# Kernel optimization log

Hardware: AMD Instinct MI355X
Metric: run time of the kernel (lower is better)

## Reference

```python
import jax, jax.numpy as jnp
import numpy as np

B, T, J, C, H = 16, 448, 448, 1024, 16
HD = C // H
NEG_INF = float('-inf')


def _layernorm(x, g, b, eps=1e-5):
    mu = jnp.mean(x, axis=-1, keepdims=True)
    var = jnp.var(x, axis=-1, keepdims=True)
    return (x - mu) * jax.lax.rsqrt(var + eps) * g + b


def _heads(x):
    # [B, S, C] -> [B, H, S, HD]
    Bv, S, _ = x.shape
    return x.reshape(Bv, S, H, HD).transpose(0, 2, 1, 3)


def _merge(x):
    # [B, H, S, HD] -> [B, S, C]
    Bv, _, S, _ = x.shape
    return x.transpose(0, 2, 1, 3).reshape(Bv, S, C)


def setup_inputs() -> dict:
    key = jax.random.key(0)
    ks = jax.random.split(key, 16)
    s = 0.02
    return {
        'tgt': jax.random.normal(ks[0], (B, T, C), jnp.float32),
        'src': jax.random.normal(ks[1], (B, J, C), jnp.float32),
        'sa_wqkv': jax.random.normal(ks[2], (C, 3 * C), jnp.float32) * s,
        'sa_wproj': jax.random.normal(ks[3], (C, C), jnp.float32) * s,
        'sa_bproj': jnp.zeros((C,), jnp.float32),
        'ed_wkv': jax.random.normal(ks[4], (C, 2 * C), jnp.float32) * s,
        'ed_wq': jax.random.normal(ks[5], (C, C), jnp.float32) * s,
        'ed_wproj': jax.random.normal(ks[6], (C, C), jnp.float32) * s,
        'ed_bproj': jnp.zeros((C,), jnp.float32),
        'ff_w1': jax.random.normal(ks[7], (C, 4 * C), jnp.float32) * s,
        'ff_b1': jnp.zeros((4 * C,), jnp.float32),
        'ff_w2': jax.random.normal(ks[8], (4 * C, C), jnp.float32) * s,
        'ff_b2': jnp.zeros((C,), jnp.float32),
        'ln1_g': jnp.ones((C,), jnp.float32), 'ln1_b': jnp.zeros((C,), jnp.float32),
        'ln2_g': jnp.ones((C,), jnp.float32), 'ln2_b': jnp.zeros((C,), jnp.float32),
        'ln3_g': jnp.ones((C,), jnp.float32), 'ln3_b': jnp.zeros((C,), jnp.float32),
        'tgt_padding_mask': jnp.zeros((B, T), bool),
    }


def _forward(tgt, src, sa_wqkv, sa_wproj, sa_bproj, ed_wkv, ed_wq, ed_wproj, ed_bproj,
             ff_w1, ff_b1, ff_w2, ff_b2, ln1_g, ln1_b, ln2_g, ln2_b, ln3_g, ln3_b,
             tgt_padding_mask):
    scale = C ** (-0.5)  # NOTE: original scales by full n_embd, not head_size

    # --- masked self-attention on ln1(tgt) ---
    x = _layernorm(tgt, ln1_g, ln1_b)
    qkv = x @ sa_wqkv
    q, k, v = (_heads(t) for t in jnp.split(qkv, 3, axis=-1))
    wei = jnp.einsum('bhtd,bhsd->bhts', q, k) * scale  # [B,H,T,T]
    causal = jnp.tril(jnp.ones((T, T), bool))
    wei = jnp.where(causal[None, None], wei, NEG_INF)
    wei = jnp.where(tgt_padding_mask[:, None, None, :], NEG_INF, wei)
    wei = jax.nn.softmax(wei, axis=-1)
    sa_out = _merge(jnp.einsum('bhts,bhsd->bhtd', wei, v)) @ sa_wproj + sa_bproj
    result = tgt + sa_out

    # --- cross-attention: ln2 applied to BOTH result and src (as in source) ---
    xq = _layernorm(result, ln2_g, ln2_b)
    xs = _layernorm(src, ln2_g, ln2_b)
    kv = xs @ ed_wkv
    k2, v2 = (_heads(t) for t in jnp.split(kv, 2, axis=-1))
    q2 = _heads(xq @ ed_wq)
    wei2 = jnp.einsum('bhtd,bhjd->bhtj', q2, k2) * scale  # [B,H,T,J]
    wei2 = jax.nn.softmax(wei2, axis=-1)
    ed_out = _merge(jnp.einsum('bhtj,bhjd->bhtd', wei2, v2)) @ ed_wproj + ed_bproj
    result = result + ed_out

    # --- FFN on ln3(tgt) (source uses tgt, not result) ---
    h = jax.nn.relu(_layernorm(tgt, ln3_g, ln3_b) @ ff_w1 + ff_b1)
    result = result + (h @ ff_w2 + ff_b2)
    return result


def reference(tgt, src, sa_wqkv, sa_wproj, sa_bproj, ed_wkv, ed_wq, ed_wproj, ed_bproj,
              ff_w1, ff_b1, ff_w2, ff_b2, ln1_g, ln1_b, ln2_g, ln2_b, ln3_g, ln3_b,
              tgt_padding_mask):
    return _forward(tgt, src, sa_wqkv, sa_wproj, sa_bproj, ed_wkv, ed_wq, ed_wproj,
                    ed_bproj, ff_w1, ff_b1, ff_w2, ff_b2, ln1_g, ln1_b, ln2_g, ln2_b,
                    ln3_g, ln3_b, tgt_padding_mask)
```

## Files before the change

kernel.cpp:

```cpp
#include <hip/hip_runtime.h>

typedef __bf16 bf16;
typedef __bf16 bf16x8 __attribute__((ext_vector_type(8)));
typedef float floatx4 __attribute__((ext_vector_type(4)));

__device__ __forceinline__ floatx4 mfma16(bf16x8 a, bf16x8 b, floatx4 c) {
    return __builtin_amdgcn_mfma_f32_16x16x32_bf16(a, b, c, 0, 0, 0);
}

__device__ __forceinline__ void load16_lds(const void* g, void* l) {
    __builtin_amdgcn_global_load_lds(
        (const __attribute__((address_space(1))) void*)g,
        (__attribute__((address_space(3))) void*)(unsigned int)(unsigned long long)l,
        16, 0, 0);
}

__global__ __launch_bounds__(256) void detect_dtype(const bf16* __restrict__ p,
                                                    int* __restrict__ flag) {
    __shared__ int bad;
    if (threadIdx.x == 0) bad = 0;
    __syncthreads();
    int lbad = 0;
    for (int i = threadIdx.x; i < 4096; i += 256) {
        const float v = (float)p[i];
        if (!isfinite(v) || fabsf(v) > 1e10f) lbad = 1;
    }
    if (lbad) atomicOr(&bad, 1);
    __syncthreads();
    if (threadIdx.x == 0) *flag = bad;
}

__global__ __launch_bounds__(256) void convert_vecs(
    const void* bpr, const void* bep, const void* fb1, const void* fb2,
    const void* g1, const void* b1, const void* g2, const void* b2,
    const void* g3, const void* b3, bf16* __restrict__ out,
    const int* __restrict__ flagp) {
    const int fl = *flagp;
    const int idx = blockIdx.x * 256 + threadIdx.x;
    const void* src;
    int off;
    if (idx < 1024)      { src = bpr; off = idx; }
    else if (idx < 2048) { src = bep; off = idx - 1024; }
    else if (idx < 6144) { src = fb1; off = idx - 2048; }
    else if (idx < 7168) { src = fb2; off = idx - 6144; }
    else {
        const void* t[6] = {g1, b1, g2, b2, g3, b3};
        src = t[(idx - 7168) >> 10];
        off = idx & 1023;
    }
    out[idx] = fl ? (bf16)((const float*)src)[off] : ((const bf16*)src)[off];
}

__global__ __launch_bounds__(256) void ln_f32(const float* __restrict__ X,
                                              const bf16* __restrict__ G,
                                              const bf16* __restrict__ Bv,
                                              bf16* __restrict__ Y) {
    const int row = blockIdx.x;
    const int tid = threadIdx.x;
    const float* x = X + (size_t)row * 1024 + tid * 4;
    float v[4];
#pragma unroll
    for (int i = 0; i < 4; i++) v[i] = x[i];
    float s = v[0] + v[1] + v[2] + v[3];
    float q = v[0] * v[0] + v[1] * v[1] + v[2] * v[2] + v[3] * v[3];
#pragma unroll
    for (int off = 32; off >= 1; off >>= 1) {
        s += __shfl_xor(s, off);
        q += __shfl_xor(q, off);
    }
    __shared__ float ss[4], qq[4];
    const int wave = tid >> 6, lane = tid & 63;
    if (lane == 0) { ss[wave] = s; qq[wave] = q; }
    __syncthreads();
    s = ss[0] + ss[1] + ss[2] + ss[3];
    q = qq[0] + qq[1] + qq[2] + qq[3];
    const float mu = s * (1.0f / 1024.0f);
    const float var = q * (1.0f / 1024.0f) - mu * mu;
    const float rs = rsqrtf(var + 1e-5f);
    bf16* y = Y + (size_t)row * 1024 + tid * 4;
    const bf16* g = G + tid * 4;
    const bf16* b = Bv + tid * 4;
#pragma unroll
    for (int i = 0; i < 4; i++)
        y[i] = (bf16)((v[i] - mu) * rs * (float)g[i] + (float)b[i]);
}

__global__ __launch_bounds__(256) void ln_dyn(const void* __restrict__ X,
                                              const bf16* __restrict__ G,
                                              const bf16* __restrict__ Bv,
                                              bf16* __restrict__ Y,
                                              const int* __restrict__ flagp) {
    const int fl = *flagp;
    const int row = blockIdx.x;
    const int tid = threadIdx.x;
    float v[4];
    if (fl) {
        const float* x = (const float*)X + (size_t)row * 1024 + tid * 4;
#pragma unroll
        for (int i = 0; i < 4; i++) v[i] = x[i];
    } else {
        const bf16* x = (const bf16*)X + (size_t)row * 1024 + tid * 4;
#pragma unroll
        for (int i = 0; i < 4; i++) v[i] = (float)x[i];
    }
    float s = v[0] + v[1] + v[2] + v[3];
    float q = v[0] * v[0] + v[1] * v[1] + v[2] * v[2] + v[3] * v[3];
#pragma unroll
    for (int off = 32; off >= 1; off >>= 1) {
        s += __shfl_xor(s, off);
        q += __shfl_xor(q, off);
    }
    __shared__ float ss[4], qq[4];
    const int wave = tid >> 6, lane = tid & 63;
    if (lane == 0) { ss[wave] = s; qq[wave] = q; }
    __syncthreads();
    s = ss[0] + ss[1] + ss[2] + ss[3];
    q = qq[0] + qq[1] + qq[2] + qq[3];
    const float mu = s * (1.0f / 1024.0f);
    const float var = q * (1.0f / 1024.0f) - mu * mu;
    const float rs = rsqrtf(var + 1e-5f);
    bf16* y = Y + (size_t)row * 1024 + tid * 4;
    const bf16* g = G + tid * 4;
    const bf16* b = Bv + tid * 4;
#pragma unroll
    for (int i = 0; i < 4; i++)
        y[i] = (bf16)((v[i] - mu) * rs * (float)g[i] + (float)b[i]);
}

__global__ __launch_bounds__(256) void transpose_all(
    const void* w0, const void* w1, const void* w2, const void* w3,
    const void* w4, const void* w5, const void* w6,
    bf16* __restrict__ out_base, const int* __restrict__ flagp) {
    const int fl = *flagp;
    const int cum[8] = {0, 3072, 4096, 6144, 7168, 8192, 12288, 16384};
    const int ntv[7] = {96, 32, 64, 32, 32, 128, 32};
    const int ldi[7] = {3072, 1024, 2048, 1024, 1024, 4096, 1024};
    const int ldo[7] = {1024, 1024, 1024, 1024, 1024, 1024, 4096};
    const size_t ooff[7] = {0, 3145728, 4194304, 6291456, 7340032, 8388608, 12582912};
    const void* ws[7] = {w0, w1, w2, w3, w4, w5, w6};

    const int g = blockIdx.x;
    int w = 0;
#pragma unroll
    for (int i = 1; i < 7; i++) if (g >= cum[i]) w = i;
    const int t = g - cum[w];
    const int xt = t % ntv[w], yt = t / ntv[w];
    const int n0 = xt * 32, k0 = yt * 32;
    const void* in = ws[w];
    bf16* out = out_base + ooff[w];
    const int ldin = ldi[w], ldout = ldo[w];

    __shared__ bf16 tile[32][33];
    const int x = threadIdx.x, y = threadIdx.y;
#pragma unroll
    for (int i = 0; i < 4; i++) {
        const size_t idx = (size_t)(k0 + y + 8 * i) * ldin + n0 + x;
        tile[y + 8 * i][x] = fl ? (bf16)((const float*)in)[idx]
                                : ((const bf16*)in)[idx];
    }
    __syncthreads();
#pragma unroll
    for (int i = 0; i < 4; i++)
        out[(size_t)(n0 + y + 8 * i) * ldout + k0 + x] = tile[x][y + 8 * i];
}

template <int TN>
__global__ __launch_bounds__(256) void gemm_bt(
    const bf16* __restrict__ A, int lda,
    const bf16* __restrict__ Bt, int ldb,
    const bf16* __restrict__ bias,
    const void* resd,
    const float* resf,
    bf16* outb, float* outf, void* dual,
    const int* __restrict__ flagp,
    int M, int N, int K, int relu) {
    constexpr int NJ = TN / 32;
    __shared__ bf16 As[128 * 32];
    __shared__ bf16 Bs[TN * 32];
    const int fl = *flagp;
    const int tid = threadIdx.x;
    const int wave = tid >> 6, lane = tid & 63;
    const int quad = lane >> 4, l16 = lane & 15;
    const int g = blockIdx.x;
    const int yb = g % 56, xb = g / 56;
    const int m0 = yb * 128, n0 = xb * TN;
    const int wm = (wave >> 1) * 64, wn = (wave & 1) * (TN / 2);
    const int srow = tid >> 2, scol = (tid & 3) * 8;

    floatx4 acc[4][NJ] = {};

    const bf16* gA = A + (size_t)(m0 + srow) * lda + scol;
    const bf16* gB = Bt + (size_t)(n0 + srow) * ldb + scol;
    const size_t a64 = (size_t)64 * lda, b64 = (size_t)64 * ldb;

    for (int k0 = 0; k0 < K; k0 += 32) {
        load16_lds(gA + k0, &As[tid * 8]);
        load16_lds(gA + k0 + a64, &As[(tid + 256) * 8]);
        load16_lds(gB + k0, &Bs[tid * 8]);
        if (TN == 128) load16_lds(gB + k0 + b64, &Bs[(tid + 256) * 8]);
        __syncthreads();
        bf16x8 af[4], bfr[NJ];
#pragma unroll
        for (int i = 0; i < 4; i++)
            af[i] = *(const bf16x8*)(&As[(wm + i * 16 + l16) * 32 + quad * 8]);
#pragma unroll
        for (int j = 0; j < NJ; j++)
            bfr[j] = *(const bf16x8*)(&Bs[(wn + j * 16 + l16) * 32 + quad * 8]);
#pragma unroll
        for (int i = 0; i < 4; i++)
#pragma unroll
            for (int j = 0; j < NJ; j++)
                acc[i][j] = mfma16(af[i], bfr[j], acc[i][j]);
        __syncthreads();
    }

#pragma unroll
    for (int i = 0; i < 4; i++) {
        const int mbase = m0 + wm + i * 16 + quad * 4;
#pragma unroll
        for (int j = 0; j < NJ; j++) {
            const int n = n0 + wn + j * 16 + l16;
            const float bv = bias ? (float)bias[n] : 0.0f;
#pragma unroll
            for (int r = 0; r < 4; r++) {
                const size_t idx = (size_t)(mbase + r) * N + n;
                float v = acc[i][j][r] + bv;
                if (relu && v < 0.0f) v = 0.0f;
                if (resd) v += fl ? ((const float*)resd)[idx]
                                  : (float)((const bf16*)resd)[idx];
                if (resf) v += resf[idx];
                if (dual) {
                    if (fl) ((float*)dual)[idx] = v;
                    else ((bf16*)dual)[idx] = (bf16)v;
                } else if (outf) {
                    outf[idx] = v;
                } else {
                    outb[idx] = (bf16)v;
                }
            }
        }
    }
}

__global__ __launch_bounds__(256) void attn_kernel(
    const bf16* __restrict__ Q, int qstride,
    const bf16* __restrict__ Kp, int kstride,
    const bf16* __restrict__ Vp, int vstride,
    bf16* __restrict__ O, int causal) {
    const int T_ = 448, HD = 64, OC = 1024;
    const float scale = 0.03125f;
    const int bh = blockIdx.y, b = bh >> 4, h = bh & 15;
    const int q0 = blockIdx.x * 32;
    const int tid = threadIdx.x, wave = tid >> 6, lane = tid & 63;
    const int quad = lane >> 4, l16 = lane & 15;

    __shared__ bf16 Pb[32][464];
    __shared__ bf16 VT[64][40];
    __shared__ float redp[32][4];
    __shared__ float Mbuf[32], Lbuf[32];

    const bf16* qb = Q + (size_t)(b * T_ + q0) * qstride + h * HD;
    const bf16* kb = Kp + (size_t)(b * T_) * kstride + h * HD;
    const bf16* vb = Vp + (size_t)(b * T_) * vstride + h * HD;

    bf16x8 qf[2][2];
#pragma unroll
    for (int qi = 0; qi < 2; qi++)
#pragma unroll
        for (int kh = 0; kh < 2; kh++)
            qf[qi][kh] = *(const bf16x8*)(qb + (size_t)(qi * 16 + l16) * qstride + kh * 32 + quad * 8);

    float S[2][7][4];
#pragma unroll
    for (int kt = 0; kt < 7; kt++) {
        const int s = wave * 112 + kt * 16 + l16;
        const bf16* kr = kb + (size_t)s * kstride + quad * 8;
        bf16x8 kf0 = *(const bf16x8*)kr;
        bf16x8 kf1 = *(const bf16x8*)(kr + 32);
#pragma unroll
        for (int qi = 0; qi < 2; qi++) {
            floatx4 c = {};
            c = mfma16(qf[qi][0], kf0, c);
            c = mfma16(qf[qi][1], kf1, c);
#pragma unroll
            for (int r = 0; r < 4; r++) {
                float v = c[r] * scale;
                if (causal) {
                    const int t = q0 + qi * 16 + quad * 4 + r;
                    if (s > t) v = -30000.0f;
                }
                S[qi][kt][r] = v;
            }
        }
    }

    float mx[2][4];
#pragma unroll
    for (int qi = 0; qi < 2; qi++)
#pragma unroll
        for (int r = 0; r < 4; r++) {
            float m = S[qi][0][r];
#pragma unroll
            for (int kt = 1; kt < 7; kt++) m = fmaxf(m, S[qi][kt][r]);
#pragma unroll
            for (int off = 1; off < 16; off <<= 1) m = fmaxf(m, __shfl_xor(m, off));
            mx[qi][r] = m;
        }
    if (l16 == 0) {
#pragma unroll
        for (int qi = 0; qi < 2; qi++)
#pragma unroll
            for (int r = 0; r < 4; r++) redp[qi * 16 + quad * 4 + r][wave] = mx[qi][r];
    }
    __syncthreads();
    if (tid < 32)
        Mbuf[tid] = fmaxf(fmaxf(redp[tid][0], redp[tid][1]),
                          fmaxf(redp[tid][2], redp[tid][3]));
    __syncthreads();

#pragma unroll
    for (int qi = 0; qi < 2; qi++)
#pragma unroll
        for (int r = 0; r < 4; r++) {
            const float Mv = Mbuf[qi * 16 + quad * 4 + r];
            float acc = 0.0f;
#pragma unroll
            for (int kt = 0; kt < 7; kt++) {
                const float p = __expf(fminf(S[qi][kt][r] - Mv, 0.0f));
                acc += p;
                Pb[qi * 16 + quad * 4 + r][wave * 112 + kt * 16 + l16] = (bf16)p;
            }
#pragma unroll
            for (int off = 1; off < 16; off <<= 1) acc += __shfl_xor(acc, off);
            if (l16 == 0) redp[qi * 16 + quad * 4 + r][wave] = acc;
        }
    __syncthreads();
    if (tid < 32)
        Lbuf[tid] = redp[tid][0] + redp[tid][1] + redp[tid][2] + redp[tid][3];

    floatx4 oacc[2] = {};
    const int qi3 = wave & 1, djb = (wave >> 1) * 2;
    for (int kt = 0; kt < 14; kt++) {
        const int s0 = kt * 32;
        const bf16* vsrc = vb + (size_t)(s0 + (tid & 31)) * vstride + (tid >> 5) * 8;
        bf16x8 vv = *(const bf16x8*)vsrc;
        __syncthreads();
#pragma unroll
        for (int e = 0; e < 8; e++) VT[(tid >> 5) * 8 + e][tid & 31] = vv[e];
        __syncthreads();
        bf16x8 pa = *(const bf16x8*)(&Pb[qi3 * 16 + l16][s0 + quad * 8]);
#pragma unroll
        for (int u = 0; u < 2; u++) {
            bf16x8 bv = *(const bf16x8*)(&VT[(djb + u) * 16 + l16][quad * 8]);
            oacc[u] = mfma16(pa, bv, oacc[u]);
        }
    }

#pragma unroll
    for (int u = 0; u < 2; u++) {
        const int d = (djb + u) * 16 + l16;
#pragma unroll
        for (int r = 0; r < 4; r++) {
            const int t = q0 + qi3 * 16 + quad * 4 + r;
            const float L = Lbuf[qi3 * 16 + quad * 4 + r];
            O[(size_t)(b * T_ + t) * OC + h * HD + d] = (bf16)(oacc[u][r] / L);
        }
    }
}

extern "C" void kernel_launch(void* const* d_in, const int* in_sizes, int n_in,
                              void* d_out, int out_size, void* d_ws, size_t ws_size,
                              hipStream_t stream) {
    const void* tgt_r  = d_in[0];
    const void* src_r  = d_in[1];
    const void* wqkv_r = d_in[2];
    const void* wpr_r  = d_in[3];
    const void* bpr_r  = d_in[4];
    const void* wkv_r  = d_in[5];
    const void* wq_r   = d_in[6];
    const void* wep_r  = d_in[7];
    const void* bep_r  = d_in[8];
    const void* fw1_r  = d_in[9];
    const void* fb1_r  = d_in[10];
    const void* fw2_r  = d_in[11];
    const void* fb2_r  = d_in[12];
    const void* l1g_r  = d_in[13];
    const void* l1b_r  = d_in[14];
    const void* l2g_r  = d_in[15];
    const void* l2b_r  = d_in[16];
    const void* l3g_r  = d_in[17];
    const void* l3b_r  = d_in[18];

    const size_t MB = 1u << 20;
    char* base = (char*)d_ws;
    bf16*  WT   = (bf16*)(base + 0 * MB);
    float* resf = (float*)(base + 32 * MB);
    bf16*  Cb   = (bf16*)(base + 60 * MB);
    bf16*  Hb   = Cb;
    bf16*  Db   = (bf16*)(base + 102 * MB);
    bf16*  x3b  = (bf16*)(base + 116 * MB);
    bf16*  vecs = (bf16*)(base + 130 * MB);
    int*   flag = (int*)(base + 130 * MB + 65536);
    bf16*  kvb  = Cb + (size_t)7168 * 1024;

    bf16* T_qkv = WT + 0;
    bf16* T_pr  = WT + 3145728;
    bf16* T_kv  = WT + 4194304;
    bf16* T_q   = WT + 6291456;
    bf16* T_ep  = WT + 7340032;
    bf16* T_f1  = WT + 8388608;
    bf16* T_f2  = WT + 12582912;

    bf16* v_bpr = vecs + 0;
    bf16* v_bep = vecs + 1024;
    bf16* v_fb1 = vecs + 2048;
    bf16* v_fb2 = vecs + 6144;
    bf16 *v_l1g = vecs + 7168,  *v_l1b = vecs + 8192;
    bf16 *v_l2g = vecs + 9216,  *v_l2b = vecs + 10240;
    bf16 *v_l3g = vecs + 11264, *v_l3b = vecs + 12288;

    const int M = 7168;
    dim3 blk(256);
    dim3 tb(32, 8);

    detect_dtype<<<1, blk, 0, stream>>>((const bf16*)tgt_r, flag);
    convert_vecs<<<52, blk, 0, stream>>>(bpr_r, bep_r, fb1_r, fb2_r, l1g_r, l1b_r,
                                         l2g_r, l2b_r, l3g_r, l3b_r, vecs, flag);
    transpose_all<<<16384, tb, 0, stream>>>(wqkv_r, wpr_r, wkv_r, wq_r, wep_r,
                                            fw1_r, fw2_r, WT, flag);

    ln_dyn<<<M, blk, 0, stream>>>(tgt_r, v_l1g, v_l1b, Db, flag);
    gemm_bt<128><<<24 * 56, blk, 0, stream>>>(
        Db, 1024, T_qkv, 1024, nullptr, nullptr, nullptr, Cb, nullptr, nullptr,
        flag, M, 3072, 1024, 0);
    attn_kernel<<<dim3(14, 256), blk, 0, stream>>>(Cb, 3072, Cb + 1024, 3072, Cb + 2048, 3072, Db, 1);
    gemm_bt<64><<<16 * 56, blk, 0, stream>>>(
        Db, 1024, T_pr, 1024, v_bpr, tgt_r, nullptr, nullptr, resf, nullptr,
        flag, M, 1024, 1024, 0);
    ln_f32<<<M, blk, 0, stream>>>(resf, v_l2g, v_l2b, Db);
    ln_dyn<<<M, blk, 0, stream>>>(src_r, v_l2g, v_l2b, Cb, flag);
    gemm_bt<128><<<16 * 56, blk, 0, stream>>>(
        Cb, 1024, T_kv, 1024, nullptr, nullptr, nullptr, kvb, nullptr, nullptr,
        flag, M, 2048, 1024, 0);
    gemm_bt<64><<<16 * 56, blk, 0, stream>>>(
        Db, 1024, T_q, 1024, nullptr, nullptr, nullptr, Cb, nullptr, nullptr,
        flag, M, 1024, 1024, 0);
    attn_kernel<<<dim3(14, 256), blk, 0, stream>>>(Cb, 1024, kvb, 2048, kvb + 1024, 2048, Db, 0);
    gemm_bt<64><<<16 * 56, blk, 0, stream>>>(
        Db, 1024, T_ep, 1024, v_bep, nullptr, resf, nullptr, resf, nullptr,
        flag, M, 1024, 1024, 0);
    ln_dyn<<<M, blk, 0, stream>>>(tgt_r, v_l3g, v_l3b, x3b, flag);
    gemm_bt<128><<<32 * 56, blk, 0, stream>>>(
        x3b, 1024, T_f1, 1024, v_fb1, nullptr, nullptr, Hb, nullptr, nullptr,
        flag, M, 4096, 1024, 1);
    gemm_bt<64><<<16 * 56, blk, 0, stream>>>(
        Hb, 4096, T_f2, 4096, v_fb2, nullptr, resf, nullptr, nullptr, d_out,
        flag, M, 1024, 4096, 0);
}
```

Before: 653.2 us.

## Replace GEMM with 256x256 double-buffered pipelined MFMA kernel

Replaces the 128-row tiled GEMM with a 512-thread kernel computing 256x256 output tiles over 64-wide K steps. It double-buffers LDS through direct global-to-LDS loads, XOR-swizzles the LDS layout and interleaves loads with MFMA quadrants under explicit barriers and priority hints. A block-index swizzle groups tiles across chiplets. The large tile aims to raise data reuse and hide memory latency. The cost is 128KB of LDS per block and only 112 blocks for the N=1024 GEMMs, which may leave many CUs idle.

```diff
diff --git a/kernel.cpp b/kernel.cpp
--- a/kernel.cpp
+++ b/kernel.cpp
@@ -164,8 +164,42 @@
         out[(size_t)(n0 + y + 8 * i) * ldout + k0 + x] = tile[x][y + 8 * i];
 }
 
-template <int TN>
-__global__ __launch_bounds__(256) void gemm_bt(
+#define G256_BARRIER do { asm volatile("" ::: "memory"); \
+    __builtin_amdgcn_s_barrier(); asm volatile("" ::: "memory"); } while (0)
+#define G256_LGKM0 do { asm volatile("s_waitcnt lgkmcnt(0)" ::: "memory"); \
+    __builtin_amdgcn_sched_barrier(0); } while (0)
+
+#define STAGE_A(T, HALF) do { \
+    const bf16* _g = aS + ((T) << 6) + (size_t)(HALF) * 128 * lda; \
+    char* _l = ldsS + (((T) & 1) << 16) + ((HALF) << 14); \
+    load16_lds(_g, _l); \
+    load16_lds(_g + (size_t)64 * lda, _l + 8192); \
+} while (0)
+#define STAGE_B(T, HALF) do { \
+    const bf16* _g = bS + ((T) << 6) + (size_t)(HALF) * 128 * ldb; \
+    char* _l = ldsS + (((T) & 1) << 16) + 32768 + ((HALF) << 14); \
+    load16_lds(_g, _l); \
+    load16_lds(_g + (size_t)64 * ldb, _l + 8192); \
+} while (0)
+
+#define DS_A(QM) do { \
+    _Pragma("unroll") for (int i = 0; i < 4; ++i) { \
+        af[i][0] = *(const bf16x8*)(Sa + ((QM) << 14) + aoff + i * 2048 + sw0); \
+        af[i][1] = *(const bf16x8*)(Sa + ((QM) << 14) + aoff + i * 2048 + (sw0 ^ 64)); \
+    } } while (0)
+#define DS_B(QN) do { \
+    _Pragma("unroll") for (int j = 0; j < 2; ++j) { \
+        bq[QN][j][0] = *(const bf16x8*)(Sb + ((QN) << 14) + boff + j * 2048 + sw0); \
+        bq[QN][j][1] = *(const bf16x8*)(Sb + ((QN) << 14) + boff + j * 2048 + (sw0 ^ 64)); \
+    } } while (0)
+#define MM(QM, QN) do { \
+    _Pragma("unroll") for (int i = 0; i < 4; ++i) \
+    _Pragma("unroll") for (int j = 0; j < 2; ++j) { \
+        acc[QM][QN][i][j] = mfma16(af[i][0], bq[QN][j][0], acc[QM][QN][i][j]); \
+        acc[QM][QN][i][j] = mfma16(af[i][1], bq[QN][j][1], acc[QM][QN][i][j]); \
+    } } while (0)
+
+__global__ __launch_bounds__(512, 2) void gemm256(
     const bf16* __restrict__ A, int lda,
     const bf16* __restrict__ Bt, int ldb,
     const bf16* __restrict__ bias,
@@ -174,69 +208,94 @@
     bf16* outb, float* outf, void* dual,
     const int* __restrict__ flagp,
     int M, int N, int K, int relu) {
-    constexpr int NJ = TN / 32;
-    __shared__ bf16 As[128 * 32];
-    __shared__ bf16 Bs[TN * 32];
+    extern __shared__ char smem[];
     const int fl = *flagp;
     const int tid = threadIdx.x;
     const int wave = tid >> 6, lane = tid & 63;
     const int quad = lane >> 4, l16 = lane & 15;
+    const int wm = wave >> 2, wn = wave & 3;
+
+    const int MT = M >> 8;
+    const int nwg = gridDim.x;
     const int g = blockIdx.x;
-    const int yb = g % 56, xb = g / 56;
-    const int m0 = yb * 128, n0 = xb * TN;
-    const int wm = (wave >> 1) * 64, wn = (wave & 1) * (TN / 2);
-    const int srow = tid >> 2, scol = (tid & 3) * 8;
-
-    floatx4 acc[4][NJ] = {};
-
-    const bf16* gA = A + (size_t)(m0 + srow) * lda + scol;
-    const bf16* gB = Bt + (size_t)(n0 + srow) * ldb + scol;
-    const size_t a64 = (size_t)64 * lda, b64 = (size_t)64 * ldb;
-
-    for (int k0 = 0; k0 < K; k0 += 32) {
-        load16_lds(gA + k0, &As[tid * 8]);
-        load16_lds(gA + k0 + a64, &As[(tid + 256) * 8]);
-        load16_lds(gB + k0, &Bs[tid * 8]);
-        if (TN == 128) load16_lds(gB + k0 + b64, &Bs[(tid + 256) * 8]);
-        __syncthreads();
-        bf16x8 af[4], bfr[NJ];
-#pragma unroll
-        for (int i = 0; i < 4; i++)
-            af[i] = *(const bf16x8*)(&As[(wm + i * 16 + l16) * 32 + quad * 8]);
-#pragma unroll
-        for (int j = 0; j < NJ; j++)
-            bfr[j] = *(const bf16x8*)(&Bs[(wn + j * 16 + l16) * 32 + quad * 8]);
-#pragma unroll
-        for (int i = 0; i < 4; i++)
-#pragma unroll
-            for (int j = 0; j < NJ; j++)
-                acc[i][j] = mfma16(af[i], bfr[j], acc[i][j]);
-        __syncthreads();
-    }
-
-#pragma unroll
-    for (int i = 0; i < 4; i++) {
-        const int mbase = m0 + wm + i * 16 + quad * 4;
-#pragma unroll
-        for (int j = 0; j < NJ; j++) {
-            const int n = n0 + wn + j * 16 + l16;
-            const float bv = bias ? (float)bias[n] : 0.0f;
-#pragma unroll
-            for (int r = 0; r < 4; r++) {
-                const size_t idx = (size_t)(mbase + r) * N + n;
-                float v = acc[i][j][r] + bv;
-                if (relu && v < 0.0f) v = 0.0f;
-                if (resd) v += fl ? ((const float*)resd)[idx]
-                                  : (float)((const bf16*)resd)[idx];
-                if (resf) v += resf[idx];
-                if (dual) {
-                    if (fl) ((float*)dual)[idx] = v;
-                    else ((bf16*)dual)[idx] = (bf16)v;
-                } else if (outf) {
-                    outf[idx] = v;
-                } else {
-                    outb[idx] = (bf16)v;
-                }
+    const int swz = (g & 7) * (nwg >> 3) + (g >> 3);
+    const int mb = swz % MT, nb = swz / MT;
+    const int m0 = mb << 8, n0 = nb << 8;
+    const int NT = K >> 6;
+
+    const int srow = tid >> 3;
+    const int sc = (tid & 7) ^ (srow & 7);
+    const bf16* aS = A + (size_t)(m0 + srow) * lda + sc * 8;
+    const bf16* bS = Bt + (size_t)(n0 + srow) * ldb + sc * 8;
+    char* ldsS = smem + tid * 16;
+
+    const int aoff = (wm * 64 + l16) * 128;
+    const int boff = (wn * 32 + l16) * 128;
+    const int sw0 = (quad * 16) ^ ((l16 & 7) << 4);
+
+    floatx4 acc[2][2][4][2] = {};
+    bf16x8 af[4][2], bq[2][2][2];
+
+    STAGE_A(0, 0); STAGE_A(0, 1); STAGE_B(0, 0); STAGE_B(0, 1);
+    STAGE_A(1, 0); STAGE_B(1, 0); STAGE_A(1, 1);
+    asm volatile("s_waitcnt vmcnt(6)" ::: "memory");
+    G256_BARRIER;
+
+    for (int t = 0; t < NT; ++t) {
+        const char* Sa = smem + ((t & 1) << 16);
+        const char* Sb = Sa + 32768;
+        DS_A(0); DS_B(0);
+        if (t + 1 < NT) STAGE_B(t + 1, 1);
+        G256_BARRIER; G256_LGKM0;
+        __builtin_amdgcn_s_setprio(1); MM(0, 0); __builtin_amdgcn_s_setprio(0);
+        G256_BARRIER;
+        DS_B(1);
+        if (t + 2 < NT) STAGE_A(t + 2, 0);
+        G256_BARRIER; G256_LGKM0;
+        __builtin_amdgcn_s_setprio(1); MM(0, 1); __builtin_amdgcn_s_setprio(0);
+        G256_BARRIER;
+        DS_A(1);
+        if (t + 2 < NT) STAGE_B(t + 2, 0);
+        G256_BARRIER; G256_LGKM0;
+        __builtin_amdgcn_s_setprio(1); MM(1, 0); __builtin_amdgcn_s_setprio(0);
+        G256_BARRIER;
+        if (t + 2 < NT) {
+            STAGE_A(t + 2, 1);
+            asm volatile("s_waitcnt vmcnt(6)" ::: "memory");
+        } else {
+            asm volatile("s_waitcnt vmcnt(0)" ::: "memory");
+        }
+        G256_BARRIER; G256_LGKM0;
+        __builtin_amdgcn_s_setprio(1); MM(1, 1); __builtin_amdgcn_s_setprio(0);
+        G256_BARRIER;
+    }
+
+#pragma unroll
+    for (int qm = 0; qm < 2; ++qm)
+#pragma unroll
+    for (int qn = 0; qn < 2; ++qn)
+#pragma unroll
+    for (int i = 0; i < 4; ++i)
+#pragma unroll
+    for (int j = 0; j < 2; ++j) {
+        const int row = m0 + qm * 128 + wm * 64 + i * 16 + quad * 4;
+        const int col = n0 + qn * 128 + wn * 32 + j * 16 + l16;
+        const float bv = bias ? (float)bias[col] : 0.0f;
+#pragma unroll
+        for (int r = 0; r < 4; ++r) {
+            const size_t idx = (size_t)(row + r) * N + col;
+            float v = acc[qm][qn][i][j][r] + bv;
+            if (relu && v < 0.0f) v = 0.0f;
+            if (resd) v += fl ? ((const float*)resd)[idx]
+                              : (float)((const bf16*)resd)[idx];
+            if (resf) v += resf[idx];
+            if (dual) {
+                if (fl) ((float*)dual)[idx] = v;
+                else ((bf16*)dual)[idx] = (bf16)v;
+            } else if (outf) {
+                outf[idx] = v;
+            } else {
+                outb[idx] = (bf16)v;
             }
         }
     }
@@ -391,6 +450,14 @@
     const void* l3g_r  = d_in[17];
     const void* l3b_r  = d_in[18];
 
+    static bool attr_done = false;
+    if (!attr_done) {
+        (void)hipFuncSetAttribute((const void*)gemm256,
+                                  hipFuncAttributeMaxDynamicSharedMemorySize,
+                                  131072);
+        attr_done = true;
+    }
+
     const size_t MB = 1u << 20;
     char* base = (char*)d_ws;
     bf16*  WT   = (bf16*)(base + 0 * MB);
@@ -421,6 +488,8 @@
 
     const int M = 7168;
     dim3 blk(256);
+    dim3 gblk(512);
+    const size_t GLDS = 131072;
     dim3 tb(32, 8);
 
     detect_dtype<<<1, blk, 0, stream>>>((const bf16*)tgt_r, flag);
@@ -430,30 +499,30 @@
                                             fw1_r, fw2_r, WT, flag);
 
     ln_dyn<<<M, blk, 0, stream>>>(tgt_r, v_l1g, v_l1b, Db, flag);
-    gemm_bt<128><<<24 * 56, blk, 0, stream>>>(
+    gemm256<<<336, gblk, GLDS, stream>>>(
         Db, 1024, T_qkv, 1024, nullptr, nullptr, nullptr, Cb, nullptr, nullptr,
         flag, M, 3072, 1024, 0);
     attn_kernel<<<dim3(14, 256), blk, 0, stream>>>(Cb, 3072, Cb + 1024, 3072, Cb + 2048, 3072, Db, 1);
-    gemm_bt<64><<<16 * 56, blk, 0, stream>>>(
+    gemm256<<<112, gblk, GLDS, stream>>>(
         Db, 1024, T_pr, 1024, v_bpr, tgt_r, nullptr, nullptr, resf, nullptr,
         flag, M, 1024, 1024, 0);
     ln_f32<<<M, blk, 0, stream>>>(resf, v_l2g, v_l2b, Db);
     ln_dyn<<<M, blk, 0, stream>>>(src_r, v_l2g, v_l2b, Cb, flag);
-    gemm_bt<128><<<16 * 56, blk, 0, stream>>>(
+    gemm256<<<224, gblk, GLDS, stream>>>(
         Cb, 1024, T_kv, 1024, nullptr, nullptr, nullptr, kvb, nullptr, nullptr,
         flag, M, 2048, 1024, 0);
-    gemm_bt<64><<<16 * 56, blk, 0, stream>>>(
+    gemm256<<<112, gblk, GLDS, stream>>>(
         Db, 1024, T_q, 1024, nullptr, nullptr, nullptr, Cb, nullptr, nullptr,
         flag, M, 1024, 1024, 0);
     attn_kernel<<<dim3(14, 256), blk, 0, stream>>>(Cb, 1024, kvb, 2048, kvb + 1024, 2048, Db, 0);
-    gemm_bt<64><<<16 * 56, blk, 0, stream>>>(
+    gemm256<<<112, gblk, GLDS, stream>>>(
         Db, 1024, T_ep, 1024, v_bep, nullptr, resf, nullptr, resf, nullptr,
         flag, M, 1024, 1024, 0);
     ln_dyn<<<M, blk, 0, stream>>>(tgt_r, v_l3g, v_l3b, x3b, flag);
-    gemm_bt<128><<<32 * 56, blk, 0, stream>>>(
+    gemm256<<<448, gblk, GLDS, stream>>>(
         x3b, 1024, T_f1, 1024, v_fb1, nullptr, nullptr, Hb, nullptr, nullptr,
         flag, M, 4096, 1024, 1);
-    gemm_bt<64><<<16 * 56, blk, 0, stream>>>(
+    gemm256<<<112, gblk, GLDS, stream>>>(
         Hb, 4096, T_f2, 4096, v_fb2, nullptr, resf, nullptr, nullptr, d_out,
         flag, M, 1024, 4096, 0);
 }
```

Result: slower. 756.2 us (+15.8%).

## Double GEMM K-tile to 64 with XOR-swizzled LDS layout

Applied to the files above, without the earlier changes.

The bf16 GEMM main loop now stages a K-slab of 64 instead of 32 per iteration, halving the number of barrier pairs per K. The LDS tile layout uses an XOR swizzle of the 16-byte column slot by row, which is meant to avoid bank conflicts on the fragment reads now that rows are 128 bytes wide. LDS use per block doubles, which may reduce occupancy, and loads are still not double-buffered.

```diff
diff --git a/kernel.cpp b/kernel.cpp
--- a/kernel.cpp
+++ b/kernel.cpp
@@ -175,8 +175,8 @@
     const int* __restrict__ flagp,
     int M, int N, int K, int relu) {
     constexpr int NJ = TN / 32;
-    __shared__ bf16 As[128 * 32];
-    __shared__ bf16 Bs[TN * 32];
+    __shared__ bf16 As[128 * 64];
+    __shared__ bf16 Bs[TN * 64];
     const int fl = *flagp;
     const int tid = threadIdx.x;
     const int wave = tid >> 6, lane = tid & 63;
@@ -185,32 +185,46 @@
     const int yb = g % 56, xb = g / 56;
     const int m0 = yb * 128, n0 = xb * TN;
     const int wm = (wave >> 1) * 64, wn = (wave & 1) * (TN / 2);
-    const int srow = tid >> 2, scol = (tid & 3) * 8;
+
+    const int srow = tid >> 3;
+    const int sc = (tid & 7) ^ (srow & 7);
+    const bf16* gA = A + (size_t)(m0 + srow) * lda + sc * 8;
+    const bf16* gB = Bt + (size_t)(n0 + srow) * ldb + sc * 8;
 
     floatx4 acc[4][NJ] = {};
 
-    const bf16* gA = A + (size_t)(m0 + srow) * lda + scol;
-    const bf16* gB = Bt + (size_t)(n0 + srow) * ldb + scol;
-    const size_t a64 = (size_t)64 * lda, b64 = (size_t)64 * ldb;
-
-    for (int k0 = 0; k0 < K; k0 += 32) {
-        load16_lds(gA + k0, &As[tid * 8]);
-        load16_lds(gA + k0 + a64, &As[(tid + 256) * 8]);
-        load16_lds(gB + k0, &Bs[tid * 8]);
-        if (TN == 128) load16_lds(gB + k0 + b64, &Bs[(tid + 256) * 8]);
+    for (int k0 = 0; k0 < K; k0 += 64) {
+#pragma unroll
+        for (int i = 0; i < 4; i++)
+            load16_lds(gA + k0 + (size_t)(32 * i) * lda, &As[tid * 8 + i * 2048]);
+#pragma unroll
+        for (int i = 0; i < TN / 32; i++)
+            load16_lds(gB + k0 + (size_t)(32 * i) * ldb, &Bs[tid * 8 + i * 2048]);
         __syncthreads();
-        bf16x8 af[4], bfr[NJ];
+        bf16x8 af[4][2], bfr[NJ][2];
 #pragma unroll
         for (int i = 0; i < 4; i++)
-            af[i] = *(const bf16x8*)(&As[(wm + i * 16 + l16) * 32 + quad * 8]);
+#pragma unroll
+            for (int h = 0; h < 2; h++) {
+                const int r = wm + i * 16 + l16;
+                const int slot = ((h << 2) + quad) ^ (r & 7);
+                af[i][h] = *(const bf16x8*)(&As[r * 64 + slot * 8]);
+            }
 #pragma unroll
         for (int j = 0; j < NJ; j++)
-            bfr[j] = *(const bf16x8*)(&Bs[(wn + j * 16 + l16) * 32 + quad * 8]);
+#pragma unroll
+            for (int h = 0; h < 2; h++) {
+                const int r = wn + j * 16 + l16;
+                const int slot = ((h << 2) + quad) ^ (r & 7);
+                bfr[j][h] = *(const bf16x8*)(&Bs[r * 64 + slot * 8]);
+            }
 #pragma unroll
         for (int i = 0; i < 4; i++)
 #pragma unroll
-            for (int j = 0; j < NJ; j++)
-                acc[i][j] = mfma16(af[i], bfr[j], acc[i][j]);
+            for (int j = 0; j < NJ; j++) {
+                acc[i][j] = mfma16(af[i][0], bfr[j][0], acc[i][j]);
+                acc[i][j] = mfma16(af[i][1], bfr[j][1], acc[i][j]);
+            }
         __syncthreads();
     }
 
```

New measurement: 624.8 us. 1.05x faster.
